# Kernel optimization log

Hardware: AMD Instinct MI355X
Metric: run time of the kernel (lower is better)

## Reference

```python
import jax, jax.numpy as jnp
import numpy as np

B, S, D = 2, 2048, 1024
H = 16
DK = D // H
FF = 4096
EPS = 1e-6


def setup_inputs() -> dict:
    key = jax.random.key(0)
    ks = jax.random.split(key, 16)
    sd = 0.02
    inp = {
        "x": jax.random.normal(ks[0], (B, S, D), dtype=jnp.float32),
        # attention projections (stored as [in, out]; y = x @ W + b)
        "Wq": jax.random.normal(ks[1], (D, D), dtype=jnp.float32) * sd,
        "bq": jnp.zeros((D,), jnp.float32),
        "Wk": jax.random.normal(ks[2], (D, D), dtype=jnp.float32) * sd,
        "bk": jnp.zeros((D,), jnp.float32),
        "Wv": jax.random.normal(ks[3], (D, D), dtype=jnp.float32) * sd,
        "bv": jnp.zeros((D,), jnp.float32),
        "Wo": jax.random.normal(ks[4], (D, D), dtype=jnp.float32) * sd,
        "bo": jnp.zeros((D,), jnp.float32),
        # FFN
        "W1": jax.random.normal(ks[5], (D, FF), dtype=jnp.float32) * sd,
        "b1": jnp.zeros((FF,), jnp.float32),
        "W2": jax.random.normal(ks[6], (FF, D), dtype=jnp.float32) * sd,
        "b2": jnp.zeros((D,), jnp.float32),
        # LayerNorms (pre-norm)
        "ln1_g": jnp.ones((D,), jnp.float32),
        "ln1_b": jnp.zeros((D,), jnp.float32),
        "ln2_g": jnp.ones((D,), jnp.float32),
        "ln2_b": jnp.zeros((D,), jnp.float32),
    }
    return inp


def _layer_norm(x, g, b):
    mu = jnp.mean(x, axis=-1, keepdims=True)
    var = jnp.mean(jnp.square(x - mu), axis=-1, keepdims=True)
    return (x - mu) * jax.lax.rsqrt(var + EPS) * g + b


def _attention(x, Wq, bq, Wk, bk, Wv, bv, Wo, bo):
    # project and split heads: [B,S,D] -> [B,H,S,DK]
    def split(t):
        return t.reshape(B, S, H, DK).transpose(0, 2, 1, 3)
    q = split(x @ Wq + bq)
    k = split(x @ Wk + bk)
    v = split(x @ Wv + bv)
    scores = jnp.einsum("bhqd,bhkd->bhqk", q, k) / jnp.sqrt(jnp.float32(DK))
    p = jax.nn.softmax(scores, axis=-1)  # no mask in forward path; dropout eval-mode
    o = jnp.einsum("bhqk,bhkd->bhqd", p, v)
    o = o.transpose(0, 2, 1, 3).reshape(B, S, D)
    return o @ Wo + bo


def reference(x, Wq, bq, Wk, bk, Wv, bv, Wo, bo, W1, b1, W2, b2,
              ln1_g, ln1_b, ln2_g, ln2_b):
    # sublayer 1: x + attn(LN(x))
    x = x + _attention(_layer_norm(x, ln1_g, ln1_b), Wq, bq, Wk, bk, Wv, bv, Wo, bo)
    # sublayer 2: x + FFN(LN(x))
    h = jax.nn.relu(_layer_norm(x, ln2_g, ln2_b) @ W1 + b1)
    x = x + (h @ W2 + b2)
    return x
```

## Files before the change

### kernel.cpp

```cpp
#include <hip/hip_runtime.h>


#define S_LEN 2048
#define DMODEL 1024
#define NHEADS 16
#define FFDIM 4096
#define MROWS 4096

typedef _Float16 f16;
typedef _Float16 f16x8 __attribute__((ext_vector_type(8)));
typedef float f32x4 __attribute__((ext_vector_type(4)));
typedef unsigned long long u64;
typedef unsigned long long u64x2 __attribute__((ext_vector_type(2)));

union Frag { f16x8 h; u64 q[2]; f16 e[8]; };

__device__ __forceinline__ f32x4 mfma16(f16x8 a, f16x8 b, f32x4 c) {
  return __builtin_amdgcn_mfma_f32_16x16x32_f16(a, b, c, 0, 0, 0);
}

typedef __attribute__((address_space(1))) const void gvoid;
typedef __attribute__((address_space(3))) void lvoid;

__device__ __forceinline__ void gload16(const f16* gp, f16* lp) {
  __builtin_amdgcn_global_load_lds((gvoid*)gp, (lvoid*)lp, 16, 0, 0);
}

__global__ __launch_bounds__(256) void wtrans_kernel(const float* __restrict__ W,
                                                     f16* __restrict__ Wt,
                                                     int K, int N) {
  __shared__ f16 tile[32][33];
  const int n0 = blockIdx.x * 32, k0 = blockIdx.y * 32;
  const int tx = threadIdx.x & 31, ty = threadIdx.x >> 5;
  for (int i = 0; i < 4; i++) {
    int k = ty + i * 8;
    tile[k][tx] = (f16)W[(size_t)(k0 + k) * N + n0 + tx];
  }
  __syncthreads();
  for (int i = 0; i < 4; i++) {
    int n = ty + i * 8;
    Wt[(size_t)(n0 + n) * K + k0 + tx] = tile[tx][n];
  }
}

__global__ void bias_concat_kernel(const float* __restrict__ bq,
                                   const float* __restrict__ bk,
                                   const float* __restrict__ bv,
                                   float* __restrict__ out) {
  int i = blockIdx.x * 256 + threadIdx.x;
  float v = (i < 1024) ? bq[i] : (i < 2048) ? bk[i - 1024] : bv[i - 2048];
  out[i] = v;
}

__global__ __launch_bounds__(256) void ln_kernel(const float* __restrict__ x,
                                                 const float* __restrict__ gw,
                                                 const float* __restrict__ bw,
                                                 f16* __restrict__ out) {
  const int row = blockIdx.x, t = threadIdx.x;
  const float* xr = x + (size_t)row * DMODEL;
  float4 v = *(const float4*)(xr + t * 4);
  float s = v.x + v.y + v.z + v.w;
  float s2 = v.x * v.x + v.y * v.y + v.z * v.z + v.w * v.w;
  for (int off = 1; off < 64; off <<= 1) {
    s += __shfl_xor(s, off);
    s2 += __shfl_xor(s2, off);
  }
  __shared__ float red[8];
  const int w = t >> 6, lane = t & 63;
  if (lane == 0) { red[w] = s; red[w + 4] = s2; }
  __syncthreads();
  s = red[0] + red[1] + red[2] + red[3];
  s2 = red[4] + red[5] + red[6] + red[7];
  float mu = s * (1.0f / DMODEL);
  float var = s2 * (1.0f / DMODEL) - mu * mu;
  float rstd = rsqrtf(var + 1e-6f);
  float4 g4 = *(const float4*)(gw + t * 4);
  float4 b4 = *(const float4*)(bw + t * 4);
  union { f16 h[4]; u64 q; } o;
  o.h[0] = (f16)((v.x - mu) * rstd * g4.x + b4.x);
  o.h[1] = (f16)((v.y - mu) * rstd * g4.y + b4.y);
  o.h[2] = (f16)((v.z - mu) * rstd * g4.z + b4.z);
  o.h[3] = (f16)((v.w - mu) * rstd * g4.w + b4.w);
  *(u64*)(out + (size_t)row * DMODEL + t * 4) = o.q;
}

template <int BM, int BN>
__global__ __launch_bounds__(256, 2) void gemm2(const f16* __restrict__ A, int lda,
                                                const f16* __restrict__ Bt, int ldb,
                                                const float* __restrict__ bias,
                                                const float* __restrict__ res,
                                                float* __restrict__ outf,
                                                f16* __restrict__ outh, int ldo,
                                                int N, int K, int relu) {
  constexpr int MT = BM / 32, NT = BN / 32;
  __shared__ f16 As[2][BM * 64];
  __shared__ f16 Bs[2][BN * 64];
  const int m0 = blockIdx.y * BM, n0 = blockIdx.x * BN;
  const int t = threadIdx.x;
  const int lane = t & 63, w = t >> 6;
  const int wr = w >> 1, wc = w & 1;
  const int rA = lane & 15, g = lane >> 4;

  f32x4 acc[MT][NT] = {};

  auto stage = [&](int k0, int buf) {
#pragma unroll
    for (int p = 0; p < BM / 32; p++) {
      const int chunk = p * 256 + w * 64 + lane;
      const int row = chunk >> 3;
      const int cbg = ((chunk & 7) ^ (row & 7)) * 8;
      gload16(A + (size_t)(m0 + row) * lda + k0 + cbg,
              &As[buf][(p * 256 + w * 64) * 8]);
    }
#pragma unroll
    for (int p = 0; p < BN / 32; p++) {
      const int chunk = p * 256 + w * 64 + lane;
      const int row = chunk >> 3;
      const int cbg = ((chunk & 7) ^ (row & 7)) * 8;
      gload16(Bt + (size_t)(n0 + row) * ldb + k0 + cbg,
              &Bs[buf][(p * 256 + w * 64) * 8]);
    }
  };

  stage(0, 0);
  int cur = 0;
  for (int k0 = 0; k0 < K; k0 += 64) {
    __syncthreads();
    if (k0 + 64 < K) stage(k0 + 64, cur ^ 1);

#pragma unroll
    for (int ks = 0; ks < 2; ks++) {
      Frag a[MT], b[NT];
#pragma unroll
      for (int mt = 0; mt < MT; mt++) {
        const int row = wr * (BM / 2) + mt * 16 + rA;
        a[mt].h = *(const f16x8*)(&As[cur][row * 64 + ((ks * 4 + g) ^ (row & 7)) * 8]);
      }
#pragma unroll
      for (int nt = 0; nt < NT; nt++) {
        const int row = wc * (BN / 2) + nt * 16 + rA;
        b[nt].h = *(const f16x8*)(&Bs[cur][row * 64 + ((ks * 4 + g) ^ (row & 7)) * 8]);
      }
#pragma unroll
      for (int mt = 0; mt < MT; mt++)
#pragma unroll
        for (int nt = 0; nt < NT; nt++)
          acc[mt][nt] = mfma16(a[mt].h, b[nt].h, acc[mt][nt]);
    }
    cur ^= 1;
  }

#pragma unroll
  for (int mt = 0; mt < MT; mt++) {
#pragma unroll
    for (int nt = 0; nt < NT; nt++) {
      const int col = n0 + wc * (BN / 2) + nt * 16 + rA;
      const int rowb = m0 + wr * (BM / 2) + mt * 16 + g * 4;
      const float bs = bias[col];
#pragma unroll
      for (int r = 0; r < 4; r++) {
        float v = acc[mt][nt][r] + bs;
        if (relu) v = fmaxf(v, 0.0f);
        if (res) v += res[(size_t)(rowb + r) * N + col];
        if (outf) outf[(size_t)(rowb + r) * N + col] = v;
        if (outh) outh[(size_t)(rowb + r) * ldo + col] = (f16)v;
      }
    }
  }
}

__global__ __launch_bounds__(256) void vtrans_kernel(const f16* __restrict__ qkv,
                                                     f16* __restrict__ vt) {
  const int bh = blockIdx.y;
  const int s0 = blockIdx.x * 64;
  const int b = bh >> 4, h = bh & 15;
  __shared__ f16 tile[64][72];
  const int t = threadIdx.x;
  for (int pass = 0; pass < 2; pass++) {
    int sl = (t >> 3) + pass * 32;
    int dk0 = (t & 7) * 8;
    u64x2 v = *(const u64x2*)(qkv + (size_t)(b * S_LEN + s0 + sl) * 3072 + 2048 + h * 64 + dk0);
    *(u64x2*)(&tile[sl][dk0]) = v;
  }
  __syncthreads();
  for (int pass = 0; pass < 2; pass++) {
    int dk = (t >> 3) + pass * 32;
    int sc = (t & 7) * 8;
    union { u64x2 q; f16 u[8]; } o;
    for (int j = 0; j < 8; j++) {
      int pos = sc + j;
      int kv = (pos & 32) | ((pos & 4) << 2) | ((pos & 0x18) >> 1) | (pos & 3);
      o.u[j] = tile[kv][dk];
    }
    *(u64x2*)(vt + (size_t)(bh * 64 + dk) * S_LEN + s0 + sc) = o.q;
  }
}

__global__ __launch_bounds__(256, 4) void attn_kernel(const f16* __restrict__ qkv,
                                                      const f16* __restrict__ vt,
                                                      f16* __restrict__ attn_out) {
  const int qt0 = blockIdx.x * 64;
  const int bh = blockIdx.y;
  const int b = bh >> 4, h = bh & 15;
  const int t = threadIdx.x;
  const int lane = t & 63, w = t >> 6;
  const int rA = lane & 15, g = lane >> 4;

  __shared__ f16 Ks[2][64 * 64];
  __shared__ f16 Vs[2][64 * 64];

  const int qrow = qt0 + w * 16 + rA;
  Frag qf[2];
#pragma unroll
  for (int kt = 0; kt < 2; kt++) {
    const f16* p = qkv + (size_t)(b * S_LEN + qrow) * 3072 + h * 64 + kt * 32 + 8 * g;
    f16x8 v = *(const f16x8*)p;
#pragma unroll
    for (int j = 0; j < 8; j++) v[j] = v[j] * (f16)0.18033688f;
    qf[kt].h = v;
  }

  float mR = -3.0e38f, lR = 0.0f;
  f32x4 o2[4] = {};

#define STAGE_KV(kv0_, buf_)                                                     \
  {                                                                              \
    _Pragma("unroll") for (int i = 0; i < 2; i++) {                              \
      int C = i * 256 + w * 64 + lane;                                           \
      int row = C >> 3;                                                          \
      int cbg = ((C & 7) ^ (row & 7)) * 8;                                       \
      gload16(qkv + (size_t)(b * S_LEN + (kv0_) + row) * 3072 + 1024 + h * 64 + cbg, \
              &Ks[buf_][(i * 256 + w * 64) * 8]);                                \
      gload16(vt + (size_t)(bh * 64 + row) * S_LEN + (kv0_) + cbg,               \
              &Vs[buf_][(i * 256 + w * 64) * 8]);                                \
    }                                                                            \
  }

  int cur = 0;
  STAGE_KV(0, 0);

  for (int kv0 = 0; kv0 < S_LEN; kv0 += 64) {
    __syncthreads();
    if (kv0 + 64 < S_LEN) STAGE_KV(kv0 + 64, cur ^ 1);

    f32x4 s[4] = {};
#pragma unroll
    for (int nt = 0; nt < 4; nt++) {
      const int row = nt * 16 + rA;
#pragma unroll
      for (int kt = 0; kt < 2; kt++) {
        Frag kf;
        kf.h = *(const f16x8*)(&Ks[cur][row * 64 + ((kt * 4 + g) ^ (row & 7)) * 8]);
        s[nt] = mfma16(kf.h, qf[kt].h, s[nt]);
      }
    }

    float mx = fmaxf(fmaxf(fmaxf(s[0][0], s[0][1]), fmaxf(s[0][2], s[0][3])),
                     fmaxf(fmaxf(s[1][0], s[1][1]), fmaxf(s[1][2], s[1][3])));
    float mx2 = fmaxf(fmaxf(fmaxf(s[2][0], s[2][1]), fmaxf(s[2][2], s[2][3])),
                      fmaxf(fmaxf(s[3][0], s[3][1]), fmaxf(s[3][2], s[3][3])));
    mx = fmaxf(mx, mx2);
    mx = fmaxf(mx, __shfl_xor(mx, 16));
    mx = fmaxf(mx, __shfl_xor(mx, 32));

    bool ok = (mx - mR <= 8.0f);
    if (!__all(ok)) {
      float mn = fmaxf(mR, mx);
      float alpha = exp2f(mR - mn);
      mR = mn;
      lR *= alpha;
#pragma unroll
      for (int ntd = 0; ntd < 4; ntd++)
#pragma unroll
        for (int r = 0; r < 4; r++) o2[ntd][r] *= alpha;
    }

    float rs = 0.0f;
#pragma unroll
    for (int nt = 0; nt < 4; nt++)
#pragma unroll
      for (int r = 0; r < 4; r++) {
        float e0 = exp2f(s[nt][r] - mR);
        s[nt][r] = e0;
        rs += e0;
      }
    rs += __shfl_xor(rs, 16);
    rs += __shfl_xor(rs, 32);
    lR += rs;

    Frag ph[2];
#pragma unroll
    for (int j = 0; j < 2; j++)
#pragma unroll
      for (int r = 0; r < 4; r++) {
        ph[j].e[r] = (f16)s[2 * j][r];
        ph[j].e[4 + r] = (f16)s[2 * j + 1][r];
      }

#pragma unroll
    for (int ntd = 0; ntd < 4; ntd++) {
      const int row = ntd * 16 + rA;
#pragma unroll
      for (int j = 0; j < 2; j++) {
        Frag vf;
        vf.h = *(const f16x8*)(&Vs[cur][row * 64 + ((j * 4 + g) ^ (row & 7)) * 8]);
        o2[ntd] = mfma16(vf.h, ph[j].h, o2[ntd]);
      }
    }

    cur ^= 1;
  }

  const float inv = 1.0f / lR;
#pragma unroll
  for (int ntd = 0; ntd < 4; ntd++) {
    union { f16 h[4]; u64 q; } pk;
#pragma unroll
    for (int r = 0; r < 4; r++) pk.h[r] = (f16)(o2[ntd][r] * inv);
    *(u64*)(attn_out + (size_t)(b * S_LEN + qrow) * DMODEL + h * 64 + ntd * 16 + g * 4) = pk.q;
  }
#undef STAGE_KV
}

extern "C" void kernel_launch(void* const* d_in, const int* in_sizes, int n_in,
                              void* d_out, int out_size, void* d_ws, size_t ws_size,
                              hipStream_t stream) {
  const float* x     = (const float*)d_in[0];
  const float* Wq    = (const float*)d_in[1];
  const float* bq    = (const float*)d_in[2];
  const float* Wk    = (const float*)d_in[3];
  const float* bk    = (const float*)d_in[4];
  const float* Wv    = (const float*)d_in[5];
  const float* bv    = (const float*)d_in[6];
  const float* Wo    = (const float*)d_in[7];
  const float* bo    = (const float*)d_in[8];
  const float* W1    = (const float*)d_in[9];
  const float* b1    = (const float*)d_in[10];
  const float* W2    = (const float*)d_in[11];
  const float* b2    = (const float*)d_in[12];
  const float* ln1g  = (const float*)d_in[13];
  const float* ln1b  = (const float*)d_in[14];
  const float* ln2g  = (const float*)d_in[15];
  const float* ln2b  = (const float*)d_in[16];
  float* out = (float*)d_out;
  char* ws = (char*)d_ws;

  size_t off = 0;
  f16* wqkv_t = (f16*)(ws + off); off += (size_t)3072 * 1024 * 2;
  f16* wo_t   = (f16*)(ws + off); off += (size_t)1024 * 1024 * 2;
  f16* w1_t   = (f16*)(ws + off); off += (size_t)4096 * 1024 * 2;
  f16* w2_t   = (f16*)(ws + off); off += (size_t)1024 * 4096 * 2;
  float* bqkv = (float*)(ws + off); off += 3072 * 4;
  f16* regB   = (f16*)(ws + off); off += (size_t)MROWS * 1024 * 2;
  f16* qkv    = (f16*)(ws + off); off += (size_t)MROWS * 3072 * 2;
  f16* vt     = (f16*)(ws + off); off += (size_t)MROWS * 1024 * 2;
  f16* hbuf   = qkv;

  wtrans_kernel<<<dim3(32, 32), 256, 0, stream>>>(Wq, wqkv_t, 1024, 1024);
  wtrans_kernel<<<dim3(32, 32), 256, 0, stream>>>(Wk, wqkv_t + (size_t)1024 * 1024, 1024, 1024);
  wtrans_kernel<<<dim3(32, 32), 256, 0, stream>>>(Wv, wqkv_t + (size_t)2048 * 1024, 1024, 1024);
  wtrans_kernel<<<dim3(32, 32), 256, 0, stream>>>(Wo, wo_t, 1024, 1024);
  wtrans_kernel<<<dim3(128, 32), 256, 0, stream>>>(W1, w1_t, 1024, 4096);
  wtrans_kernel<<<dim3(32, 128), 256, 0, stream>>>(W2, w2_t, 4096, 1024);
  bias_concat_kernel<<<12, 256, 0, stream>>>(bq, bk, bv, bqkv);

  ln_kernel<<<MROWS, 256, 0, stream>>>(x, ln1g, ln1b, regB);

  gemm2<128, 128><<<dim3(24, 32), 256, 0, stream>>>(regB, 1024, wqkv_t, 1024, bqkv,
                                                    nullptr, nullptr, qkv, 3072,
                                                    3072, 1024, 0);
  vtrans_kernel<<<dim3(32, 32), 256, 0, stream>>>(qkv, vt);

  attn_kernel<<<dim3(32, 32), 256, 0, stream>>>(qkv, vt, regB);

  gemm2<128, 64><<<dim3(16, 32), 256, 0, stream>>>(regB, 1024, wo_t, 1024, bo,
                                                   x, out, nullptr, 0,
                                                   1024, 1024, 0);
  ln_kernel<<<MROWS, 256, 0, stream>>>(out, ln2g, ln2b, regB);

  gemm2<128, 128><<<dim3(32, 32), 256, 0, stream>>>(regB, 1024, w1_t, 1024, b1,
                                                    nullptr, nullptr, hbuf, 4096,
                                                    4096, 1024, 1);
  gemm2<128, 64><<<dim3(16, 32), 256, 0, stream>>>(hbuf, 4096, w2_t, 4096, b2,
                                                   out, out, nullptr, 0,
                                                   1024, 4096, 0);
}
```

Baseline: 298.4 us.

## Split A/B tile staging and hand-schedule the GEMM prefetch pipeline

The single stage() prefetch in gemm2 becomes separate stageA/stageB loads with explicit s_waitcnt vmcnt/lgkmcnt and raw s_barrier calls. The A tile is prefetched one step further ahead, and the B load is issued right before the compute of the current buffer. The goal is better overlap of global-to-LDS loads with MFMA work and a looser barrier schedule. It depends on the hard-coded vmcnt(4) matching the number of A loads per stage, which ties correctness to the tile sizes.

After: 295.2 us. About the same (-1.1%).

```diff
diff --git a/kernel.cpp b/kernel.cpp
--- a/kernel.cpp
+++ b/kernel.cpp
@@ -103,7 +103,7 @@
 
   f32x4 acc[MT][NT] = {};
 
-  auto stage = [&](int k0, int buf) {
+  auto stageA = [&](int k0, int buf) {
 #pragma unroll
     for (int p = 0; p < BM / 32; p++) {
       const int chunk = p * 256 + w * 64 + lane;
@@ -112,6 +112,8 @@
       gload16(A + (size_t)(m0 + row) * lda + k0 + cbg,
               &As[buf][(p * 256 + w * 64) * 8]);
     }
+  };
+  auto stageB = [&](int k0, int buf) {
 #pragma unroll
     for (int p = 0; p < BN / 32; p++) {
       const int chunk = p * 256 + w * 64 + lane;
@@ -122,12 +124,7 @@
     }
   };
 
-  stage(0, 0);
-  int cur = 0;
-  for (int k0 = 0; k0 < K; k0 += 64) {
-    __syncthreads();
-    if (k0 + 64 < K) stage(k0 + 64, cur ^ 1);
-
+  auto compute = [&](int cur) {
 #pragma unroll
     for (int ks = 0; ks < 2; ks++) {
       Frag a[MT], b[NT];
@@ -147,8 +144,29 @@
         for (int nt = 0; nt < NT; nt++)
           acc[mt][nt] = mfma16(a[mt].h, b[nt].h, acc[mt][nt]);
     }
-    cur ^= 1;
-  }
+  };
+
+  const int nsteps = K / 64;
+  stageA(0, 0);
+  stageB(0, 0);
+  stageA(64, 1);
+
+  for (int ts = 0; ts < nsteps - 1; ++ts) {
+    const int cur = ts & 1;
+    asm volatile("s_waitcnt vmcnt(4)" ::: "memory");
+    __builtin_amdgcn_sched_barrier(0);
+    __builtin_amdgcn_s_barrier();
+    stageB(ts * 64 + 64, cur ^ 1);
+    compute(cur);
+    asm volatile("s_waitcnt lgkmcnt(0)" ::: "memory");
+    __builtin_amdgcn_sched_barrier(0);
+    __builtin_amdgcn_s_barrier();
+    if (ts + 2 < nsteps) stageA(ts * 64 + 128, cur);
+  }
+  asm volatile("s_waitcnt vmcnt(0)" ::: "memory");
+  __builtin_amdgcn_sched_barrier(0);
+  __builtin_amdgcn_s_barrier();
+  compute((nsteps - 1) & 1);
 
 #pragma unroll
   for (int mt = 0; mt < MT; mt++) {
```

## Use triple-buffered K=32 GEMM pipeline with explicit vmcnt waits and merged weight transposes

Applied to the files above, without the earlier changes.

Rewrites the GEMM main loop into a three-stage LDS ring with 32-wide K slices. Explicit s_waitcnt vmcnt counts let two tiles of loads stay in flight while the current one is computed, and occupancy is raised to 3 blocks per CU. The Wo and W2 GEMMs switch from 128x64 to 128x128 tiles, which halves their grid to 256 blocks and may underfill the CUs. The four 1024x1024 weight transposes are also merged into one launch to save launch overhead.

Result: slower. 338.2 us (+13.4%).

```diff
diff --git a/kernel.cpp b/kernel.cpp
--- a/kernel.cpp
+++ b/kernel.cpp
@@ -40,6 +40,31 @@
   for (int i = 0; i < 4; i++) {
     int n = ty + i * 8;
     Wt[(size_t)(n0 + n) * K + k0 + tx] = tile[tx][n];
+  }
+}
+
+__global__ __launch_bounds__(256) void wtrans4_kernel(const float* __restrict__ W0,
+                                                      const float* __restrict__ W1,
+                                                      const float* __restrict__ W2,
+                                                      const float* __restrict__ W3,
+                                                      f16* __restrict__ D0,
+                                                      f16* __restrict__ D1,
+                                                      f16* __restrict__ D2,
+                                                      f16* __restrict__ D3) {
+  const int z = blockIdx.z;
+  const float* W = z == 0 ? W0 : z == 1 ? W1 : z == 2 ? W2 : W3;
+  f16* Wt = z == 0 ? D0 : z == 1 ? D1 : z == 2 ? D2 : D3;
+  __shared__ f16 tile[32][33];
+  const int n0 = blockIdx.x * 32, k0 = blockIdx.y * 32;
+  const int tx = threadIdx.x & 31, ty = threadIdx.x >> 5;
+  for (int i = 0; i < 4; i++) {
+    int k = ty + i * 8;
+    tile[k][tx] = (f16)W[(size_t)(k0 + k) * 1024 + n0 + tx];
+  }
+  __syncthreads();
+  for (int i = 0; i < 4; i++) {
+    int n = ty + i * 8;
+    Wt[(size_t)(n0 + n) * 1024 + k0 + tx] = tile[tx][n];
   }
 }
 
@@ -85,7 +110,7 @@
 }
 
 template <int BM, int BN>
-__global__ __launch_bounds__(256, 2) void gemm2(const f16* __restrict__ A, int lda,
+__global__ __launch_bounds__(256, 3) void gemm3(const f16* __restrict__ A, int lda,
                                                 const f16* __restrict__ Bt, int ldb,
                                                 const float* __restrict__ bias,
                                                 const float* __restrict__ res,
@@ -93,8 +118,8 @@
                                                 f16* __restrict__ outh, int ldo,
                                                 int N, int K, int relu) {
   constexpr int MT = BM / 32, NT = BN / 32;
-  __shared__ f16 As[2][BM * 64];
-  __shared__ f16 Bs[2][BN * 64];
+  __shared__ f16 As[3][BM * 32];
+  __shared__ f16 Bs[3][BN * 32];
   const int m0 = blockIdx.y * BM, n0 = blockIdx.x * BN;
   const int t = threadIdx.x;
   const int lane = t & 63, w = t >> 6;
@@ -103,51 +128,66 @@
 
   f32x4 acc[MT][NT] = {};
 
-  auto stage = [&](int k0, int buf) {
-#pragma unroll
-    for (int p = 0; p < BM / 32; p++) {
-      const int chunk = p * 256 + w * 64 + lane;
-      const int row = chunk >> 3;
-      const int cbg = ((chunk & 7) ^ (row & 7)) * 8;
+  auto stage = [&](int ts, int buf) {
+    const int k0 = ts * 32;
+#pragma unroll
+    for (int p = 0; p < BM / 64; p++) {
+      const int chunk = p * 256 + t;
+      const int row = chunk >> 2;
+      const int cbg = ((chunk & 3) ^ (row & 3)) * 8;
       gload16(A + (size_t)(m0 + row) * lda + k0 + cbg,
               &As[buf][(p * 256 + w * 64) * 8]);
     }
 #pragma unroll
-    for (int p = 0; p < BN / 32; p++) {
-      const int chunk = p * 256 + w * 64 + lane;
-      const int row = chunk >> 3;
-      const int cbg = ((chunk & 7) ^ (row & 7)) * 8;
+    for (int p = 0; p < BN / 64; p++) {
+      const int chunk = p * 256 + t;
+      const int row = chunk >> 2;
+      const int cbg = ((chunk & 3) ^ (row & 3)) * 8;
       gload16(Bt + (size_t)(n0 + row) * ldb + k0 + cbg,
               &Bs[buf][(p * 256 + w * 64) * 8]);
     }
   };
 
+  auto compute = [&](int buf) {
+    Frag a[MT], b[NT];
+#pragma unroll
+    for (int mt = 0; mt < MT; mt++) {
+      const int row = wr * (BM / 2) + mt * 16 + rA;
+      a[mt].h = *(const f16x8*)(&As[buf][row * 32 + ((g ^ (row & 3)) * 8)]);
+    }
+#pragma unroll
+    for (int nt = 0; nt < NT; nt++) {
+      const int row = wc * (BN / 2) + nt * 16 + rA;
+      b[nt].h = *(const f16x8*)(&Bs[buf][row * 32 + ((g ^ (row & 3)) * 8)]);
+    }
+#pragma unroll
+    for (int mt = 0; mt < MT; mt++)
+#pragma unroll
+      for (int nt = 0; nt < NT; nt++)
+        acc[mt][nt] = mfma16(a[mt].h, b[nt].h, acc[mt][nt]);
+  };
+
+  const int nsteps = K / 32;
   stage(0, 0);
+  stage(1, 1);
+  stage(2, 2);
+
   int cur = 0;
-  for (int k0 = 0; k0 < K; k0 += 64) {
-    __syncthreads();
-    if (k0 + 64 < K) stage(k0 + 64, cur ^ 1);
-
-#pragma unroll
-    for (int ks = 0; ks < 2; ks++) {
-      Frag a[MT], b[NT];
-#pragma unroll
-      for (int mt = 0; mt < MT; mt++) {
-        const int row = wr * (BM / 2) + mt * 16 + rA;
-        a[mt].h = *(const f16x8*)(&As[cur][row * 64 + ((ks * 4 + g) ^ (row & 7)) * 8]);
-      }
-#pragma unroll
-      for (int nt = 0; nt < NT; nt++) {
-        const int row = wc * (BN / 2) + nt * 16 + rA;
-        b[nt].h = *(const f16x8*)(&Bs[cur][row * 64 + ((ks * 4 + g) ^ (row & 7)) * 8]);
-      }
-#pragma unroll
-      for (int mt = 0; mt < MT; mt++)
-#pragma unroll
-        for (int nt = 0; nt < NT; nt++)
-          acc[mt][nt] = mfma16(a[mt].h, b[nt].h, acc[mt][nt]);
-    }
-    cur ^= 1;
+  for (int ts = 0; ts < nsteps; ++ts) {
+    if (ts < nsteps - 2)
+      asm volatile("s_waitcnt vmcnt(8)" ::: "memory");
+    else if (ts == nsteps - 2)
+      asm volatile("s_waitcnt vmcnt(4)" ::: "memory");
+    else
+      asm volatile("s_waitcnt vmcnt(0)" ::: "memory");
+    __builtin_amdgcn_sched_barrier(0);
+    __builtin_amdgcn_s_barrier();
+    compute(cur);
+    asm volatile("s_waitcnt lgkmcnt(0)" ::: "memory");
+    __builtin_amdgcn_sched_barrier(0);
+    __builtin_amdgcn_s_barrier();
+    if (ts + 3 < nsteps) stage(ts + 3, cur);
+    cur = (cur == 2) ? 0 : cur + 1;
   }
 
 #pragma unroll
@@ -356,32 +396,31 @@
   f16* vt     = (f16*)(ws + off); off += (size_t)MROWS * 1024 * 2;
   f16* hbuf   = qkv;
 
-  wtrans_kernel<<<dim3(32, 32), 256, 0, stream>>>(Wq, wqkv_t, 1024, 1024);
-  wtrans_kernel<<<dim3(32, 32), 256, 0, stream>>>(Wk, wqkv_t + (size_t)1024 * 1024, 1024, 1024);
-  wtrans_kernel<<<dim3(32, 32), 256, 0, stream>>>(Wv, wqkv_t + (size_t)2048 * 1024, 1024, 1024);
-  wtrans_kernel<<<dim3(32, 32), 256, 0, stream>>>(Wo, wo_t, 1024, 1024);
+  wtrans4_kernel<<<dim3(32, 32, 4), 256, 0, stream>>>(
+      Wq, Wk, Wv, Wo,
+      wqkv_t, wqkv_t + (size_t)1024 * 1024, wqkv_t + (size_t)2048 * 1024, wo_t);
   wtrans_kernel<<<dim3(128, 32), 256, 0, stream>>>(W1, w1_t, 1024, 4096);
   wtrans_kernel<<<dim3(32, 128), 256, 0, stream>>>(W2, w2_t, 4096, 1024);
   bias_concat_kernel<<<12, 256, 0, stream>>>(bq, bk, bv, bqkv);
 
   ln_kernel<<<MROWS, 256, 0, stream>>>(x, ln1g, ln1b, regB);
 
-  gemm2<128, 128><<<dim3(24, 32), 256, 0, stream>>>(regB, 1024, wqkv_t, 1024, bqkv,
+  gemm3<128, 128><<<dim3(24, 32), 256, 0, stream>>>(regB, 1024, wqkv_t, 1024, bqkv,
                                                     nullptr, nullptr, qkv, 3072,
                                                     3072, 1024, 0);
   vtrans_kernel<<<dim3(32, 32), 256, 0, stream>>>(qkv, vt);
 
   attn_kernel<<<dim3(32, 32), 256, 0, stream>>>(qkv, vt, regB);
 
-  gemm2<128, 64><<<dim3(16, 32), 256, 0, stream>>>(regB, 1024, wo_t, 1024, bo,
+  gemm3<128, 128><<<dim3(8, 32), 256, 0, stream>>>(regB, 1024, wo_t, 1024, bo,
                                                    x, out, nullptr, 0,
                                                    1024, 1024, 0);
   ln_kernel<<<MROWS, 256, 0, stream>>>(out, ln2g, ln2b, regB);
 
-  gemm2<128, 128><<<dim3(32, 32), 256, 0, stream>>>(regB, 1024, w1_t, 1024, b1,
+  gemm3<128, 128><<<dim3(32, 32), 256, 0, stream>>>(regB, 1024, w1_t, 1024, b1,
                                                     nullptr, nullptr, hbuf, 4096,
                                                     4096, 1024, 1);
-  gemm2<128, 64><<<dim3(16, 32), 256, 0, stream>>>(hbuf, 4096, w2_t, 4096, b2,
+  gemm3<128, 128><<<dim3(8, 32), 256, 0, stream>>>(hbuf, 4096, w2_t, 4096, b2,
                                                    out, out, nullptr, 0,
                                                    1024, 4096, 0);
 }
```
